# Kernel optimization log

Measured on AMD Instinct MI355X. Metric: run time of the kernel, lower is better.

The kernel has to match this reference:

```python
import jax, jax.numpy as jnp
import numpy as np

V, D, H, HS, BLK, L = 50257, 768, 12, 64, 1024, 6
B, S = 4, 1024
EPS = 1e-5


def layer_norm(x, g, b):
    mu = jnp.mean(x, axis=-1, keepdims=True)
    var = jnp.mean(jnp.square(x - mu), axis=-1, keepdims=True)
    return (x - mu) * jax.lax.rsqrt(var + EPS) * g + b


def setup_inputs() -> dict:
    key = jax.random.key(0)
    ks = jax.random.split(key, 24)
    s = 0.02
    inp = {
        "idx": jax.random.randint(ks[0], (B, S), 0, V),
        "tok_emb": jax.random.normal(ks[1], (V, D), jnp.float32) * s,
        "pos_emb": jax.random.normal(ks[2], (BLK, D), jnp.float32) * s,
        "Wq": jax.random.normal(ks[3], (L, H, D, HS), jnp.float32) * s,
        "bq": jnp.zeros((L, H, HS), jnp.float32),
        "Wk": jax.random.normal(ks[4], (L, H, D, HS), jnp.float32) * s,
        "bk": jnp.zeros((L, H, HS), jnp.float32),
        "Wv": jax.random.normal(ks[5], (L, H, D, HS), jnp.float32) * s,
        "bv": jnp.zeros((L, H, HS), jnp.float32),
        "Wproj": jax.random.normal(ks[6], (L, D, D), jnp.float32) * s,
        "bproj": jnp.zeros((L, D), jnp.float32),
        "ln1_g": jnp.ones((L, D), jnp.float32),
        "ln1_b": jnp.zeros((L, D), jnp.float32),
        "ln2_g": jnp.ones((L, D), jnp.float32),
        "ln2_b": jnp.zeros((L, D), jnp.float32),
        "Wf1": jax.random.normal(ks[7], (L, D, 4 * D), jnp.float32) * s,
        "bf1": jnp.zeros((L, 4 * D), jnp.float32),
        "Wf2": jax.random.normal(ks[8], (L, 4 * D, D), jnp.float32) * s,
        "bf2": jnp.zeros((L, D), jnp.float32),
        "lnf_g": jnp.ones((D,), jnp.float32),
        "lnf_b": jnp.zeros((D,), jnp.float32),
        "Wlm": jax.random.normal(ks[9], (V, D), jnp.float32) * s,
    }
    return inp


def attention(x, Wq, bq, Wk, bk, Wv, bv, Wproj, bproj):
    # x: [B,S,D]; per-head projections stacked over H
    q = jnp.einsum("bsd,hdk->bhsk", x, Wq) + bq[:, None, :]
    k = jnp.einsum("bsd,hdk->bhsk", x, Wk) + bk[:, None, :]
    v = jnp.einsum("bsd,hdk->bhsk", x, Wv) + bv[:, None, :]
    scores = jnp.einsum("bhsk,bhtk->bhst", q, k)  # [B,H,S,S]
    s = x.shape[1]
    mask = jnp.tril(jnp.ones((s, s), bool))
    # original: masked_fill(-inf) THEN divide by sqrt(head_size) -- equivalent
    scores = jnp.where(mask, scores, -jnp.inf) / np.sqrt(HS)
    w = jax.nn.softmax(scores, axis=-1)
    out = jnp.einsum("bhst,bhtk->bhsk", w, v)
    out = out.transpose(0, 2, 1, 3).reshape(x.shape[0], s, H * HS)
    return out @ Wproj + bproj


def reference(idx, tok_emb, pos_emb, Wq, bq, Wk, bk, Wv, bv, Wproj, bproj,
              ln1_g, ln1_b, ln2_g, ln2_b, Wf1, bf1, Wf2, bf2, lnf_g, lnf_b, Wlm):
    s = idx.shape[1]
    x = tok_emb[idx] + pos_emb[:s]
    for i in range(L):
        h = layer_norm(x, ln1_g[i], ln1_b[i])
        x = x + attention(h, Wq[i], bq[i], Wk[i], bk[i], Wv[i], bv[i], Wproj[i], bproj[i])
        h = layer_norm(x, ln2_g[i], ln2_b[i])
        x = x + (jax.nn.gelu(h @ Wf1[i] + bf1[i], approximate=False) @ Wf2[i] + bf2[i])
    x = layer_norm(x, lnf_g, lnf_b)
    logits = x @ Wlm.T  # [B,S,V]
    return logits
```

## Files before the change

kernel.cpp:

```cpp
#include <hip/hip_runtime.h>
#include <hip/hip_bf16.h>
#include <math.h>

#define D_MODEL 768
#define N_HEAD  12
#define HEAD    64
#define SEQ     1024
#define NLAYER  6
#define BATCH   4
#define NROWS   (BATCH*SEQ)
#define VOCAB   50257
#define VPAD    50432
#define DFFN    3072
#define DQKV    2304

typedef __attribute__((ext_vector_type(8))) __bf16 bf16x8;
typedef __attribute__((ext_vector_type(4))) float f32x4;
typedef __attribute__((ext_vector_type(4))) unsigned short u16x4;
typedef __attribute__((ext_vector_type(8))) unsigned short u16x8;

__device__ inline unsigned short f2bf(float x) {
    __hip_bfloat16 h = __float2bfloat16(x);
    return *reinterpret_cast<unsigned short*>(&h);
}

__global__ __launch_bounds__(256)
void embed_kernel(const int* __restrict__ idx, const float* __restrict__ tok,
                  const float* __restrict__ pos, float* __restrict__ x) {
    int row = blockIdx.x;
    int t = idx[row];
    int s = row & (SEQ - 1);
    const float* tp = tok + (size_t)t * D_MODEL;
    const float* pp = pos + (size_t)s * D_MODEL;
    float* xp = x + (size_t)row * D_MODEL;
    for (int i = threadIdx.x; i < D_MODEL; i += 256) xp[i] = tp[i] + pp[i];
}

__global__ __launch_bounds__(256)
void ln_kernel(const float* __restrict__ in, const float* __restrict__ gw,
               const float* __restrict__ bw, unsigned short* __restrict__ out) {
    int row = blockIdx.x;
    int tid = threadIdx.x;
    const float* x = in + (size_t)row * D_MODEL;
    float v0 = x[tid], v1 = x[tid + 256], v2 = x[tid + 512];
    float s  = v0 + v1 + v2;
    float sq = v0*v0 + v1*v1 + v2*v2;
    #pragma unroll
    for (int o = 1; o < 64; o <<= 1) { s += __shfl_xor(s, o); sq += __shfl_xor(sq, o); }
    __shared__ float red[8];
    int wave = tid >> 6;
    if ((tid & 63) == 0) { red[wave] = s; red[4 + wave] = sq; }
    __syncthreads();
    s  = red[0] + red[1] + red[2] + red[3];
    sq = red[4] + red[5] + red[6] + red[7];
    float mean = s * (1.0f / D_MODEL);
    float var  = sq * (1.0f / D_MODEL) - mean * mean;
    float rstd = rsqrtf(var + 1e-5f);
    unsigned short* op = out + (size_t)row * D_MODEL;
    op[tid]       = f2bf((v0 - mean) * rstd * gw[tid]       + bw[tid]);
    op[tid + 256] = f2bf((v1 - mean) * rstd * gw[tid + 256] + bw[tid + 256]);
    op[tid + 512] = f2bf((v2 - mean) * rstd * gw[tid + 512] + bw[tid + 512]);
}

template<int MODE>
__global__ __launch_bounds__(256)
void conv_transpose(const float* __restrict__ in, unsigned short* __restrict__ out,
                    int K, int N, size_t inLstride, size_t outLstride) {
    __shared__ float t[64][65];
    const int tid = threadIdx.x;
    const int n0 = blockIdx.x * 64, k0 = blockIdx.y * 64;
    const float* ip = in + blockIdx.z * inLstride;
    unsigned short* op = out + blockIdx.z * outLstride;
    {
        const int kk = tid >> 4, nq = tid & 15;
        #pragma unroll
        for (int p = 0; p < 4; ++p) {
            int k = kk + p * 16;
            float4 v;
            if (MODE == 0) v = *reinterpret_cast<const float4*>(&ip[(size_t)(k0 + k) * N + n0 + nq * 4]);
            else           v = *reinterpret_cast<const float4*>(&ip[((size_t)(n0 >> 6) * K + (k0 + k)) * 64 + nq * 4]);
            t[k][nq * 4 + 0] = v.x; t[k][nq * 4 + 1] = v.y;
            t[k][nq * 4 + 2] = v.z; t[k][nq * 4 + 3] = v.w;
        }
    }
    __syncthreads();
    {
        const int n = tid >> 2, kq = tid & 3;
        unsigned short buf[16];
        #pragma unroll
        for (int j = 0; j < 16; ++j) buf[j] = f2bf(t[kq * 16 + j][n]);
        unsigned short* dst = &op[(size_t)(n0 + n) * K + k0 + kq * 16];
        *reinterpret_cast<u16x8*>(dst)     = *reinterpret_cast<u16x8*>(&buf[0]);
        *reinterpret_cast<u16x8*>(dst + 8) = *reinterpret_cast<u16x8*>(&buf[8]);
    }
}

__global__ __launch_bounds__(256)
void conv_lm(const float* __restrict__ in, unsigned short* __restrict__ out) {
    const int nchunks = VPAD * D_MODEL / 4;
    const int vchunks = VOCAB * D_MODEL / 4;
    for (int i = blockIdx.x * 256 + threadIdx.x; i < nchunks; i += gridDim.x * 256) {
        u16x4 o;
        if (i < vchunks) {
            float4 v = reinterpret_cast<const float4*>(in)[i];
            o[0] = f2bf(v.x); o[1] = f2bf(v.y); o[2] = f2bf(v.z); o[3] = f2bf(v.w);
        } else { o[0] = 0; o[1] = 0; o[2] = 0; o[3] = 0; }
        reinterpret_cast<u16x4*>(out)[i] = o;
    }
}

__global__ __launch_bounds__(256)
void conv_bias(const float* __restrict__ bq, const float* __restrict__ bk,
               const float* __restrict__ bv, float* __restrict__ out) {
    int i = blockIdx.x * 256 + threadIdx.x;
    if (i >= NLAYER * DQKV) return;
    int l = i / DQKV, n = i % DQKV;
    float v;
    if (n < 768)        v = bq[l * 768 + n];
    else if (n < 1536)  v = bk[l * 768 + n - 768];
    else                v = bv[l * 768 + n - 1536];
    out[i] = v;
}

__global__ __launch_bounds__(512)
void gemm256_mfma(const unsigned short* __restrict__ A, const unsigned short* __restrict__ B,
                  float* __restrict__ C, int M, int N, int K) {
    __shared__ unsigned short smem[2 * 16384];
    const int nwg = gridDim.x;
    const int t0 = (blockIdx.x & 7) * (nwg >> 3) + (blockIdx.x >> 3);
    const int MT = M >> 8;
    const int NBX = nwg / MT;
    const int srsize = NBX * 8;
    const int sr = t0 / srsize;
    const int rem = t0 - sr * srsize;
    const int bx = rem >> 3;
    const int by = sr * 8 + (rem & 7);
    const int bm = by * 256, bn = bx * 256;
    const int tid = threadIdx.x;
    const int l = tid & 63, w = tid >> 6;
    const int wm = w >> 2, wn = w & 3;
    const int lr = l & 15, lc = l >> 4;
    f32x4 acc[8][4] = {};

    auto stage = [&](int k0, int buf) {
        #pragma unroll
        for (int p = 0; p < 2; ++p) {
            int d16 = p * 512 + tid;
            int row = d16 >> 2, cph = d16 & 3;
            int clog = cph ^ (row & 3);
            const unsigned short* ga = A + (size_t)(bm + row) * K + k0 + clog * 8;
            __builtin_amdgcn_global_load_lds(
                (const __attribute__((address_space(1))) unsigned int*)ga,
                (__attribute__((address_space(3))) unsigned int*)(&smem[buf * 16384 + d16 * 8]), 16, 0, 0);
        }
        #pragma unroll
        for (int p = 0; p < 2; ++p) {
            int d16 = p * 512 + tid;
            int row = d16 >> 2, cph = d16 & 3;
            int clog = cph ^ (row & 3);
            const unsigned short* gb = B + (size_t)(bn + row) * K + k0 + clog * 8;
            __builtin_amdgcn_global_load_lds(
                (const __attribute__((address_space(1))) unsigned int*)gb,
                (__attribute__((address_space(3))) unsigned int*)(&smem[buf * 16384 + 8192 + d16 * 8]), 16, 0, 0);
        }
    };

    auto compute = [&](int buf) {
        const unsigned short* Ab = &smem[buf * 16384];
        const unsigned short* Bb = &smem[buf * 16384 + 8192];
        #pragma unroll
        for (int qm = 0; qm < 2; ++qm) {
            bf16x8 af[4];
            #pragma unroll
            for (int mi = 0; mi < 4; ++mi) {
                int row = wm * 128 + qm * 64 + mi * 16 + lr;
                af[mi] = *reinterpret_cast<const bf16x8*>(&Ab[row * 32 + ((lc ^ (row & 3)) * 8)]);
            }
            #pragma unroll
            for (int qn = 0; qn < 2; ++qn) {
                bf16x8 bfr[2];
                #pragma unroll
                for (int ni = 0; ni < 2; ++ni) {
                    int col = wn * 64 + qn * 32 + ni * 16 + lr;
                    bfr[ni] = *reinterpret_cast<const bf16x8*>(&Bb[col * 32 + ((lc ^ (col & 3)) * 8)]);
                }
                __builtin_amdgcn_s_setprio(1);
                #pragma unroll
                for (int mi = 0; mi < 4; ++mi)
                    #pragma unroll
                    for (int ni = 0; ni < 2; ++ni)
                        acc[qm * 4 + mi][qn * 2 + ni] = __builtin_amdgcn_mfma_f32_16x16x32_bf16(
                            af[mi], bfr[ni], acc[qm * 4 + mi][qn * 2 + ni], 0, 0, 0);
                __builtin_amdgcn_s_setprio(0);
            }
        }
    };

    const int NT = K >> 5;
    stage(0, 0);
    asm volatile("s_waitcnt vmcnt(0)" ::: "memory");
    __builtin_amdgcn_s_barrier();
    for (int t = 0; t < NT; ++t) {
        const int cur = t & 1;
        if (t + 1 < NT) stage((t + 1) << 5, cur ^ 1);
        compute(cur);
        if (t + 1 < NT) {
            asm volatile("s_waitcnt vmcnt(0)" ::: "memory");
            __builtin_amdgcn_s_barrier();
        }
    }

    #pragma unroll
    for (int i = 0; i < 8; ++i) {
        #pragma unroll
        for (int r = 0; r < 4; ++r) {
            const int row = bm + wm * 128 + i * 16 + lc * 4 + r;
            #pragma unroll
            for (int j = 0; j < 4; ++j) {
                const int col = bn + wn * 64 + j * 16 + lr;
                if (col < N) C[(size_t)row * N + col] = acc[i][j][r];
            }
        }
    }
}

template<int BM, int OUTF , bool GELU, bool RES>
__global__ __launch_bounds__(256)
void gemm_sched(const unsigned short* __restrict__ A, const unsigned short* __restrict__ B,
                const float* __restrict__ bias, const float* __restrict__ res,
                void* __restrict__ Cout, int M, int N, int K) {
    constexpr int ABUF = BM * 64;
    constexpr int TBUF = (BM + 128) * 64;
    __shared__ unsigned short smem[2 * TBUF];
    const int nwg = gridDim.x;
    const int t0 = (blockIdx.x & 7) * (nwg >> 3) + (blockIdx.x >> 3);
    const int MT = M / BM;
    const int NBX = nwg / MT;
    const int srsize = NBX * 8;
    const int sr = t0 / srsize;
    const int rem = t0 - sr * srsize;
    const int bx = rem >> 3;
    const int by = sr * 8 + (rem & 7);
    const int bm = by * BM, bn = bx * 128;
    const int tid = threadIdx.x;
    const int l = tid & 63, w = tid >> 6;
    constexpr int MI = (BM == 128) ? 4 : 2;
    const int wr = (BM == 128) ? (w >> 1) * 64 : (w & 1) * 32;
    const int wc = (BM == 128) ? (w & 1) * 64 : (w >> 1) * 64;
    const int lr = l & 15, lc = l >> 4;
    f32x4 acc[MI][4] = {};

    auto stage = [&](int k0, int buf) {
        #pragma unroll
        for (int p = 0; p < BM * 8 / 256; ++p) {
            int d16 = p * 256 + tid;
            int row = d16 >> 3, cph = d16 & 7;
            int clog = cph ^ (row & 7);
            const unsigned short* ga = A + (size_t)(bm + row) * K + k0 + clog * 8;
            __builtin_amdgcn_global_load_lds(
                (const __attribute__((address_space(1))) unsigned int*)ga,
                (__attribute__((address_space(3))) unsigned int*)(&smem[buf * TBUF + d16 * 8]), 16, 0, 0);
        }
        #pragma unroll
        for (int p = 0; p < 4; ++p) {
            int d16 = p * 256 + tid;
            int row = d16 >> 3, cph = d16 & 7;
            int clog = cph ^ (row & 7);
            const unsigned short* gb = B + (size_t)(bn + row) * K + k0 + clog * 8;
            __builtin_amdgcn_global_load_lds(
                (const __attribute__((address_space(1))) unsigned int*)gb,
                (__attribute__((address_space(3))) unsigned int*)(&smem[buf * TBUF + ABUF + d16 * 8]), 16, 0, 0);
        }
    };

    auto compute = [&](int buf) {
        const unsigned short* Ab = &smem[buf * TBUF];
        const unsigned short* Bb = &smem[buf * TBUF + ABUF];
        #pragma unroll
        for (int ks = 0; ks < 2; ++ks) {
            bf16x8 af[MI], bfr[4];
            #pragma unroll
            for (int mi = 0; mi < MI; ++mi) {
                int row = wr + mi * 16 + lr;
                af[mi] = *reinterpret_cast<const bf16x8*>(
                    &Ab[row * 64 + (((ks * 4 + lc) ^ (row & 7)) * 8)]);
            }
            #pragma unroll
            for (int ni = 0; ni < 4; ++ni) {
                int col = wc + ni * 16 + lr;
                bfr[ni] = *reinterpret_cast<const bf16x8*>(
                    &Bb[col * 64 + (((ks * 4 + lc) ^ (col & 7)) * 8)]);
            }
            __builtin_amdgcn_s_setprio(1);
            #pragma unroll
            for (int mi = 0; mi < MI; ++mi)
                #pragma unroll
                for (int ni = 0; ni < 4; ++ni)
                    acc[mi][ni] = __builtin_amdgcn_mfma_f32_16x16x32_bf16(
                        bfr[ni], af[mi], acc[mi][ni], 0, 0, 0);
            __builtin_amdgcn_s_setprio(0);
        }
    };

    const int NT = K >> 6;
    stage(0, 0);
    asm volatile("s_waitcnt vmcnt(0)" ::: "memory");
    __builtin_amdgcn_s_barrier();
    for (int t = 0; t < NT; ++t) {
        const int cur = t & 1;
        if (t + 1 < NT) stage((t + 1) << 6, cur ^ 1);
        compute(cur);
        if (t + 1 < NT) {
            asm volatile("s_waitcnt vmcnt(0)" ::: "memory");
            __builtin_amdgcn_s_barrier();
        }
    }

    #pragma unroll
    for (int mi = 0; mi < MI; ++mi) {
        const int row = bm + wr + mi * 16 + lr;
        #pragma unroll
        for (int ni = 0; ni < 4; ++ni) {
            const int colb = bn + wc + ni * 16 + lc * 4;
            f32x4 v = acc[mi][ni];
            if (bias) v += *reinterpret_cast<const f32x4*>(&bias[colb]);
            if (GELU) {
                #pragma unroll
                for (int r = 0; r < 4; ++r)
                    v[r] = 0.5f * v[r] * (1.0f + erff(v[r] * 0.70710678118654752f));
            }
            if (RES) v += *reinterpret_cast<const f32x4*>(&res[(size_t)row * N + colb]);
            if (OUTF == 0) {
                *reinterpret_cast<f32x4*>(&((float*)Cout)[(size_t)row * N + colb]) = v;
            } else {
                u16x4 o;
                o[0] = f2bf(v[0]); o[1] = f2bf(v[1]); o[2] = f2bf(v[2]); o[3] = f2bf(v[3]);
                *reinterpret_cast<u16x4*>(&((unsigned short*)Cout)[(size_t)row * N + colb]) = o;
            }
        }
    }
}

__global__ __launch_bounds__(512)
void attn_mfma(const unsigned short* __restrict__ qkv, unsigned short* __restrict__ ao) {
    const int qt = gridDim.x - 1 - blockIdx.x;
    const int h = blockIdx.y, b = blockIdx.z;
    const int tid = threadIdx.x;
    const int w = tid >> 6, l = tid & 63;
    const int c = l & 15, g = l >> 4;

    __shared__ unsigned short Ks[32 * 64];
    __shared__ unsigned short Vt[64 * 40];
    __shared__ unsigned int   Ps[8][16 * 20];

    const unsigned short* base = qkv + (size_t)(b * SEQ) * DQKV + h * HEAD;
    const int q0 = qt * 128 + w * 16;

    bf16x8 qf[2];
    {
        const unsigned short* qp = base + (size_t)(q0 + c) * DQKV + g * 8;
        qf[0] = *reinterpret_cast<const bf16x8*>(qp);
        qf[1] = *reinterpret_cast<const bf16x8*>(qp + 32);
    }

    f32x4 o_acc[4] = {};
    float m_run[4]  = {-INFINITY, -INFINITY, -INFINITY, -INFINITY};
    float l_run[4]  = {0.f, 0.f, 0.f, 0.f};

    const int srow = tid >> 4, sch8 = tid & 15;
    const int scj = sch8 >> 1, sh = sch8 & 1;
    const int vd = tid & 63, vw = tid >> 6;

    const int nkt = 4 * qt + 4;
    for (int kt = 0; kt < nkt; ++kt) {
        {
            const unsigned short* kp = base + (size_t)(kt * 32 + srow) * DQKV + 768 + sch8 * 4;
            u16x4 kv = *reinterpret_cast<const u16x4*>(kp);
            *reinterpret_cast<u16x4*>(&Ks[srow * 64 + ((scj ^ (srow & 7)) * 8) + sh * 4]) = kv;
        }
        {
            unsigned short vv[4];
            #pragma unroll
            for (int j = 0; j < 4; ++j)
                vv[j] = base[(size_t)(kt * 32 + vw * 4 + j) * DQKV + 1536 + vd];
            uint2 pk;
            pk.x = vv[0] | ((unsigned)vv[1] << 16);
            pk.y = vv[2] | ((unsigned)vv[3] << 16);
            *reinterpret_cast<uint2*>(&Vt[vd * 40 + vw * 4]) = pk;
        }
        __syncthreads();

        f32x4 s_acc[2] = {};
        #pragma unroll
        for (int t = 0; t < 2; ++t) {
            const int kr = t * 16 + c;
            #pragma unroll
            for (int ks = 0; ks < 2; ++ks) {
                bf16x8 kf = *reinterpret_cast<const bf16x8*>(
                    &Ks[kr * 64 + (((ks * 4 + g) ^ (kr & 7)) * 8)]);
                s_acc[t] = __builtin_amdgcn_mfma_f32_16x16x32_bf16(qf[ks], kf, s_acc[t], 0, 0, 0);
            }
        }
        float sc[2][4];
        #pragma unroll
        for (int t = 0; t < 2; ++t) {
            const int kglob = kt * 32 + t * 16 + c;
            #pragma unroll
            for (int r = 0; r < 4; ++r) {
                float v = s_acc[t][r] * 0.125f;
                sc[t][r] = (kglob > q0 + g * 4 + r) ? -1e30f : v;
            }
        }
        float pout[2][4];
        #pragma unroll
        for (int r = 0; r < 4; ++r) {
            float tmax = fmaxf(sc[0][r], sc[1][r]);
            #pragma unroll
            for (int ms = 1; ms < 16; ms <<= 1) tmax = fmaxf(tmax, __shfl_xor(tmax, ms));
            float mnew = fmaxf(m_run[r], tmax);
            float alpha = __expf(m_run[r] - mnew);
            float p0 = __expf(sc[0][r] - mnew);
            float p1 = __expf(sc[1][r] - mnew);
            float psum = p0 + p1;
            #pragma unroll
            for (int ms = 1; ms < 16; ms <<= 1) psum += __shfl_xor(psum, ms);
            l_run[r] = l_run[r] * alpha + psum;
            m_run[r] = mnew;
            #pragma unroll
            for (int dt = 0; dt < 4; ++dt) o_acc[dt][r] *= alpha;
            pout[0][r] = p0; pout[1][r] = p1;
        }
        #pragma unroll
        for (int t = 0; t < 2; ++t) {
            #pragma unroll
            for (int r = 0; r < 4; ++r) {
                int my = f2bf(pout[t][r]);
                int part = __shfl_xor(my, 1);
                unsigned int word = (c & 1) ? ((unsigned)(part & 0xffff) | ((unsigned)my << 16))
                                            : ((unsigned)(my & 0xffff) | ((unsigned)part << 16));
                Ps[w][(g * 4 + r) * 20 + t * 8 + (c >> 1)] = word;
            }
        }
        uint4 praw = *reinterpret_cast<const uint4*>(&Ps[w][c * 20 + g * 4]);
        bf16x8 pf = *reinterpret_cast<const bf16x8*>(&praw);
        #pragma unroll
        for (int dt = 0; dt < 4; ++dt) {
            bf16x8 vf = *reinterpret_cast<const bf16x8*>(&Vt[(dt * 16 + c) * 40 + g * 8]);
            o_acc[dt] = __builtin_amdgcn_mfma_f32_16x16x32_bf16(pf, vf, o_acc[dt], 0, 0, 0);
        }
        __syncthreads();
    }

    float inv[4];
    #pragma unroll
    for (int r = 0; r < 4; ++r) inv[r] = 1.0f / l_run[r];
    #pragma unroll
    for (int r = 0; r < 4; ++r) {
        unsigned short* op = ao + (size_t)(b * SEQ + q0 + g * 4 + r) * D_MODEL + h * HEAD + c;
        #pragma unroll
        for (int dt = 0; dt < 4; ++dt)
            op[dt * 16] = f2bf(o_acc[dt][r] * inv[r]);
    }
}

extern "C" void kernel_launch(void* const* d_in, const int* in_sizes, int n_in,
                              void* d_out, int out_size, void* d_ws, size_t ws_size,
                              hipStream_t stream) {
    const int*   idx     = (const int*)  d_in[0];
    const float* tok_emb = (const float*)d_in[1];
    const float* pos_emb = (const float*)d_in[2];
    const float* Wq      = (const float*)d_in[3];
    const float* bq      = (const float*)d_in[4];
    const float* Wk      = (const float*)d_in[5];
    const float* bk      = (const float*)d_in[6];
    const float* Wv      = (const float*)d_in[7];
    const float* bv      = (const float*)d_in[8];
    const float* Wproj   = (const float*)d_in[9];
    const float* bproj   = (const float*)d_in[10];
    const float* ln1g    = (const float*)d_in[11];
    const float* ln1b    = (const float*)d_in[12];
    const float* ln2g    = (const float*)d_in[13];
    const float* ln2b    = (const float*)d_in[14];
    const float* Wf1     = (const float*)d_in[15];
    const float* bf1     = (const float*)d_in[16];
    const float* Wf2     = (const float*)d_in[17];
    const float* bf2     = (const float*)d_in[18];
    const float* lnfg    = (const float*)d_in[19];
    const float* lnfb    = (const float*)d_in[20];
    const float* Wlm     = (const float*)d_in[21];
    float* outp = (float*)d_out;

    char* basep = (char*)d_ws;
    size_t off = 0;
    auto alloc = [&](size_t bytes) -> void* {
        void* p = basep + off;
        off = (off + bytes + 255) & ~(size_t)255;
        return p;
    };
    float*          x      = (float*)         alloc((size_t)NROWS * D_MODEL * 4);
    unsigned short* qkv    = (unsigned short*)alloc((size_t)NROWS * DQKV * 2);
    unsigned short* hb     = (unsigned short*)alloc((size_t)NROWS * D_MODEL * 2);
    unsigned short* ao     = (unsigned short*)alloc((size_t)NROWS * D_MODEL * 2);
    unsigned short* mid    = (unsigned short*)alloc((size_t)NROWS * DFFN * 2);
    unsigned short* Wqkvb  = (unsigned short*)alloc((size_t)NLAYER * DQKV * D_MODEL * 2);
    unsigned short* Wprojb = (unsigned short*)alloc((size_t)NLAYER * D_MODEL * D_MODEL * 2);
    unsigned short* Wf1b   = (unsigned short*)alloc((size_t)NLAYER * DFFN * D_MODEL * 2);
    unsigned short* Wf2b   = (unsigned short*)alloc((size_t)NLAYER * D_MODEL * DFFN * 2);
    unsigned short* Wlmb   = (unsigned short*)alloc((size_t)VPAD * D_MODEL * 2);
    float*          bqkv   = (float*)         alloc((size_t)NLAYER * DQKV * 4);

    dim3 blk(256);

    conv_lm<<<2048, blk, 0, stream>>>(Wlm, Wlmb);
    conv_transpose<1><<<dim3(12, 12, 6), blk, 0, stream>>>(Wq, Wqkvb,             768, 768,  (size_t)768*768,  (size_t)DQKV*768);
    conv_transpose<1><<<dim3(12, 12, 6), blk, 0, stream>>>(Wk, Wqkvb + 768*768,   768, 768,  (size_t)768*768,  (size_t)DQKV*768);
    conv_transpose<1><<<dim3(12, 12, 6), blk, 0, stream>>>(Wv, Wqkvb + 2*768*768, 768, 768,  (size_t)768*768,  (size_t)DQKV*768);
    conv_transpose<0><<<dim3(12, 12, 6), blk, 0, stream>>>(Wproj, Wprojb,         768, 768,  (size_t)768*768,  (size_t)768*768);
    conv_transpose<0><<<dim3(48, 12, 6), blk, 0, stream>>>(Wf1, Wf1b,             768, 3072, (size_t)768*3072, (size_t)3072*768);
    conv_transpose<0><<<dim3(12, 48, 6), blk, 0, stream>>>(Wf2, Wf2b,             3072, 768, (size_t)3072*768, (size_t)768*3072);
    conv_bias<<<(NLAYER * DQKV + 255) / 256, blk, 0, stream>>>(bq, bk, bv, bqkv);

    embed_kernel<<<NROWS, blk, 0, stream>>>(idx, tok_emb, pos_emb, x);

    dim3 gqkv(32 * 18);
    dim3 g768s(64 * 6);
    dim3 g3072(32 * 24);
    dim3 ga(SEQ / 128, N_HEAD, BATCH);

    for (int li = 0; li < NLAYER; ++li) {
        ln_kernel<<<NROWS, blk, 0, stream>>>(x, ln1g + li * D_MODEL, ln1b + li * D_MODEL, hb);

        gemm_sched<128, 1, false, false><<<gqkv, blk, 0, stream>>>(
            hb, Wqkvb + (size_t)li * DQKV * D_MODEL, bqkv + li * DQKV, nullptr,
            qkv, NROWS, DQKV, D_MODEL);

        attn_mfma<<<ga, dim3(512), 0, stream>>>(qkv, ao);

        gemm_sched<64, 0, false, true><<<g768s, blk, 0, stream>>>(
            ao, Wprojb + (size_t)li * D_MODEL * D_MODEL, bproj + li * D_MODEL, x,
            x, NROWS, D_MODEL, D_MODEL);

        ln_kernel<<<NROWS, blk, 0, stream>>>(x, ln2g + li * D_MODEL, ln2b + li * D_MODEL, hb);

        gemm_sched<128, 1, true, false><<<g3072, blk, 0, stream>>>(
            hb, Wf1b + (size_t)li * DFFN * D_MODEL, bf1 + li * DFFN, nullptr,
            mid, NROWS, DFFN, D_MODEL);

        gemm_sched<64, 0, false, true><<<g768s, blk, 0, stream>>>(
            mid, Wf2b + (size_t)li * D_MODEL * DFFN, bf2 + li * D_MODEL, x,
            x, NROWS, D_MODEL, DFFN);
    }

    ln_kernel<<<NROWS, blk, 0, stream>>>(x, lnfg, lnfb, hb);

    dim3 gl((VPAD / 256) * (NROWS / 256));
    gemm256_mfma<<<gl, dim3(512), 0, stream>>>(hb, Wlmb, outp, NROWS, VOCAB, D_MODEL);
}
```

Measured before the change: 2.122 ms.

## Deepen GEMM K-tile to 64 and double-buffer attention K/V with register prefetch

The 256x256 MFMA GEMM now stages 64-wide K slices instead of 32, with an 8-way XOR swizzle. This halves the number of barrier and wait rounds per GEMM but doubles LDS use to 128 KB per block. The attention kernel double-buffers its K and V shared tiles and prefetches the next tile into registers after the barrier. That lets the global loads overlap compute and removes the trailing __syncthreads. The cost is higher register and LDS pressure, which may reduce occupancy.

```diff
diff --git a/kernel.cpp b/kernel.cpp
--- a/kernel.cpp
+++ b/kernel.cpp
@@ -125,7 +125,7 @@
 __global__ __launch_bounds__(512)
 void gemm256_mfma(const unsigned short* __restrict__ A, const unsigned short* __restrict__ B,
                   float* __restrict__ C, int M, int N, int K) {
-    __shared__ unsigned short smem[2 * 16384];
+    __shared__ unsigned short smem[2 * 2 * 16384];
     const int nwg = gridDim.x;
     const int t0 = (blockIdx.x & 7) * (nwg >> 3) + (blockIdx.x >> 3);
     const int MT = M >> 8;
@@ -144,65 +144,73 @@
 
     auto stage = [&](int k0, int buf) {
         #pragma unroll
-        for (int p = 0; p < 2; ++p) {
+        for (int p = 0; p < 4; ++p) {
             int d16 = p * 512 + tid;
-            int row = d16 >> 2, cph = d16 & 3;
-            int clog = cph ^ (row & 3);
+            int row = d16 >> 3, cph = d16 & 7;
+            int clog = cph ^ (row & 7);
             const unsigned short* ga = A + (size_t)(bm + row) * K + k0 + clog * 8;
             __builtin_amdgcn_global_load_lds(
                 (const __attribute__((address_space(1))) unsigned int*)ga,
-                (__attribute__((address_space(3))) unsigned int*)(&smem[buf * 16384 + d16 * 8]), 16, 0, 0);
-        }
-        #pragma unroll
-        for (int p = 0; p < 2; ++p) {
+                (__attribute__((address_space(3))) unsigned int*)(&smem[buf * 32768 + d16 * 8]), 16, 0, 0);
+        }
+        #pragma unroll
+        for (int p = 0; p < 4; ++p) {
             int d16 = p * 512 + tid;
-            int row = d16 >> 2, cph = d16 & 3;
-            int clog = cph ^ (row & 3);
+            int row = d16 >> 3, cph = d16 & 7;
+            int clog = cph ^ (row & 7);
             const unsigned short* gb = B + (size_t)(bn + row) * K + k0 + clog * 8;
             __builtin_amdgcn_global_load_lds(
                 (const __attribute__((address_space(1))) unsigned int*)gb,
-                (__attribute__((address_space(3))) unsigned int*)(&smem[buf * 16384 + 8192 + d16 * 8]), 16, 0, 0);
+                (__attribute__((address_space(3))) unsigned int*)(&smem[buf * 32768 + 16384 + d16 * 8]), 16, 0, 0);
         }
     };
 
     auto compute = [&](int buf) {
-        const unsigned short* Ab = &smem[buf * 16384];
-        const unsigned short* Bb = &smem[buf * 16384 + 8192];
+        const unsigned short* Ab = &smem[buf * 32768];
+        const unsigned short* Bb = &smem[buf * 32768 + 16384];
         #pragma unroll
         for (int qm = 0; qm < 2; ++qm) {
-            bf16x8 af[4];
-            #pragma unroll
-            for (int mi = 0; mi < 4; ++mi) {
-                int row = wm * 128 + qm * 64 + mi * 16 + lr;
-                af[mi] = *reinterpret_cast<const bf16x8*>(&Ab[row * 32 + ((lc ^ (row & 3)) * 8)]);
-            }
+            bf16x8 af[2][4];
+            #pragma unroll
+            for (int ks = 0; ks < 2; ++ks)
+                #pragma unroll
+                for (int mi = 0; mi < 4; ++mi) {
+                    int row = wm * 128 + qm * 64 + mi * 16 + lr;
+                    af[ks][mi] = *reinterpret_cast<const bf16x8*>(
+                        &Ab[row * 64 + (((ks * 4 + lc) ^ (row & 7)) * 8)]);
+                }
             #pragma unroll
             for (int qn = 0; qn < 2; ++qn) {
-                bf16x8 bfr[2];
+                bf16x8 bfr[2][2];
                 #pragma unroll
-                for (int ni = 0; ni < 2; ++ni) {
-                    int col = wn * 64 + qn * 32 + ni * 16 + lr;
-                    bfr[ni] = *reinterpret_cast<const bf16x8*>(&Bb[col * 32 + ((lc ^ (col & 3)) * 8)]);
-                }
+                for (int ks = 0; ks < 2; ++ks)
+                    #pragma unroll
+                    for (int ni = 0; ni < 2; ++ni) {
+                        int col = wn * 64 + qn * 32 + ni * 16 + lr;
+                        bfr[ks][ni] = *reinterpret_cast<const bf16x8*>(
+                            &Bb[col * 64 + (((ks * 4 + lc) ^ (col & 7)) * 8)]);
+                    }
                 __builtin_amdgcn_s_setprio(1);
                 #pragma unroll
-                for (int mi = 0; mi < 4; ++mi)
+                for (int ks = 0; ks < 2; ++ks)
                     #pragma unroll
-                    for (int ni = 0; ni < 2; ++ni)
-                        acc[qm * 4 + mi][qn * 2 + ni] = __builtin_amdgcn_mfma_f32_16x16x32_bf16(
-                            af[mi], bfr[ni], acc[qm * 4 + mi][qn * 2 + ni], 0, 0, 0);
+                    for (int mi = 0; mi < 4; ++mi)
+                        #pragma unroll
+                        for (int ni = 0; ni < 2; ++ni)
+                            acc[qm * 4 + mi][qn * 2 + ni] = __builtin_amdgcn_mfma_f32_16x16x32_bf16(
+                                af[ks][mi], bfr[ks][ni], acc[qm * 4 + mi][qn * 2 + ni], 0, 0, 0);
                 __builtin_amdgcn_s_setprio(0);
             }
         }
     };
 
-    const int NT = K >> 5;
+    const int NT = K >> 6;
     stage(0, 0);
     asm volatile("s_waitcnt vmcnt(0)" ::: "memory");
     __builtin_amdgcn_s_barrier();
     for (int t = 0; t < NT; ++t) {
         const int cur = t & 1;
-        if (t + 1 < NT) stage((t + 1) << 5, cur ^ 1);
+        if (t + 1 < NT) stage((t + 1) << 6, cur ^ 1);
         compute(cur);
         if (t + 1 < NT) {
             asm volatile("s_waitcnt vmcnt(0)" ::: "memory");
@@ -349,8 +357,8 @@
     const int w = tid >> 6, l = tid & 63;
     const int c = l & 15, g = l >> 4;
 
-    __shared__ unsigned short Ks[32 * 64];
-    __shared__ unsigned short Vt[64 * 40];
+    __shared__ unsigned short Ks[2][32 * 64];
+    __shared__ unsigned short Vt[2][64 * 40];
     __shared__ unsigned int   Ps[8][16 * 20];
 
     const unsigned short* base = qkv + (size_t)(b * SEQ) * DQKV + h * HEAD;
@@ -371,24 +379,29 @@
     const int scj = sch8 >> 1, sh = sch8 & 1;
     const int vd = tid & 63, vw = tid >> 6;
 
+    u16x4 kreg;
+    unsigned short vreg[4];
+    auto loadKV = [&](int kt) {
+        kreg = *reinterpret_cast<const u16x4*>(
+            base + (size_t)(kt * 32 + srow) * DQKV + 768 + sch8 * 4);
+        #pragma unroll
+        for (int j = 0; j < 4; ++j)
+            vreg[j] = base[(size_t)(kt * 32 + vw * 4 + j) * DQKV + 1536 + vd];
+    };
+
     const int nkt = 4 * qt + 4;
+    loadKV(0);
     for (int kt = 0; kt < nkt; ++kt) {
+        const int bf = kt & 1;
+        *reinterpret_cast<u16x4*>(&Ks[bf][srow * 64 + ((scj ^ (srow & 7)) * 8) + sh * 4]) = kreg;
         {
-            const unsigned short* kp = base + (size_t)(kt * 32 + srow) * DQKV + 768 + sch8 * 4;
-            u16x4 kv = *reinterpret_cast<const u16x4*>(kp);
-            *reinterpret_cast<u16x4*>(&Ks[srow * 64 + ((scj ^ (srow & 7)) * 8) + sh * 4]) = kv;
-        }
-        {
-            unsigned short vv[4];
-            #pragma unroll
-            for (int j = 0; j < 4; ++j)
-                vv[j] = base[(size_t)(kt * 32 + vw * 4 + j) * DQKV + 1536 + vd];
             uint2 pk;
-            pk.x = vv[0] | ((unsigned)vv[1] << 16);
-            pk.y = vv[2] | ((unsigned)vv[3] << 16);
-            *reinterpret_cast<uint2*>(&Vt[vd * 40 + vw * 4]) = pk;
+            pk.x = vreg[0] | ((unsigned)vreg[1] << 16);
+            pk.y = vreg[2] | ((unsigned)vreg[3] << 16);
+            *reinterpret_cast<uint2*>(&Vt[bf][vd * 40 + vw * 4]) = pk;
         }
         __syncthreads();
+        if (kt + 1 < nkt) loadKV(kt + 1);
 
         f32x4 s_acc[2] = {};
         #pragma unroll
@@ -397,7 +410,7 @@
             #pragma unroll
             for (int ks = 0; ks < 2; ++ks) {
                 bf16x8 kf = *reinterpret_cast<const bf16x8*>(
-                    &Ks[kr * 64 + (((ks * 4 + g) ^ (kr & 7)) * 8)]);
+                    &Ks[bf][kr * 64 + (((ks * 4 + g) ^ (kr & 7)) * 8)]);
                 s_acc[t] = __builtin_amdgcn_mfma_f32_16x16x32_bf16(qf[ks], kf, s_acc[t], 0, 0, 0);
             }
         }
@@ -445,10 +458,9 @@
         bf16x8 pf = *reinterpret_cast<const bf16x8*>(&praw);
         #pragma unroll
         for (int dt = 0; dt < 4; ++dt) {
-            bf16x8 vf = *reinterpret_cast<const bf16x8*>(&Vt[(dt * 16 + c) * 40 + g * 8]);
+            bf16x8 vf = *reinterpret_cast<const bf16x8*>(&Vt[bf][(dt * 16 + c) * 40 + g * 8]);
             o_acc[dt] = __builtin_amdgcn_mfma_f32_16x16x32_bf16(pf, vf, o_acc[dt], 0, 0, 0);
         }
-        __syncthreads();
     }
 
     float inv[4];
```

After: 2.034 ms. -4.2%, faster.
